# Kernel optimization log

Measured on AMD Instinct MI355X. Metric: run time of the kernel, lower is better.

The kernel has to match this reference:

```python
import jax, jax.numpy as jnp
import numpy as np

B = 8192
NUM_NODES = 100000
EMB = 128
W1D, W2D, W3D = 64, 128, 256   # witness_dims
CODE = 128
HID = 64                        # hardcoded hidden_dim in WitnessExtractor / decoder
TOTW = W1D + W2D + W3D          # 448


def _linear_params(key, fan_in, fan_out):
    k1, k2 = jax.random.split(key)
    bound = 1.0 / np.sqrt(fan_in)
    w = jax.random.uniform(k1, (fan_out, fan_in), jnp.float32, -bound, bound)
    b = jax.random.uniform(k2, (fan_out,), jnp.float32, -bound, bound)
    return w, b


def setup_inputs() -> dict:
    key = jax.random.key(0)
    ks = jax.random.split(key, 12)
    u = jax.random.randint(ks[0], (B,), 0, NUM_NODES, dtype=jnp.int64 if jax.config.jax_enable_x64 else jnp.int32)
    v = jax.random.randint(ks[1], (B,), 0, NUM_NODES, dtype=u.dtype)
    emb = jax.random.normal(ks[2], (NUM_NODES, EMB), jnp.float32)
    e1_w1, e1_b1 = _linear_params(ks[3], 2 * EMB, HID)
    e1_w2, e1_b2 = _linear_params(ks[4], HID, W1D)
    e2_w1, e2_b1 = _linear_params(ks[5], 2 * EMB + W1D, HID)
    e2_w2, e2_b2 = _linear_params(ks[6], HID, W2D)
    e3_w1, e3_b1 = _linear_params(ks[7], 2 * EMB + W2D, HID)
    e3_w2, e3_b2 = _linear_params(ks[8], HID, W3D)
    trop_w = jax.random.normal(ks[9], (CODE, TOTW), jnp.float32)  # init_scale=1.0
    dec_w1, dec_b1 = _linear_params(ks[10], CODE, HID)
    dec_w2, dec_b2 = _linear_params(ks[11], HID, 1)
    return dict(u=u, v=v, emb=emb,
                e1_w1=e1_w1, e1_b1=e1_b1, e1_w2=e1_w2, e1_b2=e1_b2,
                e2_w1=e2_w1, e2_b1=e2_b1, e2_w2=e2_w2, e2_b2=e2_b2,
                e3_w1=e3_w1, e3_b1=e3_b1, e3_w2=e3_w2, e3_b2=e3_b2,
                trop_w=trop_w, dec_w1=dec_w1, dec_b1=dec_b1,
                dec_w2=dec_w2, dec_b2=dec_b2)


def _witness(x, w1, b1, w2, b2):
    h = jax.nn.relu(x @ w1.T + b1)
    return jax.nn.sigmoid(h @ w2.T + b2)


def reference(u, v, emb,
              e1_w1, e1_b1, e1_w2, e1_b2,
              e2_w1, e2_b1, e2_w2, e2_b2,
              e3_w1, e3_b1, e3_w2, e3_b2,
              trop_w, dec_w1, dec_b1, dec_w2, dec_b2):
    u_emb = emb[u]                               # [B, EMB]
    v_emb = emb[v]
    base = jnp.concatenate([u_emb, v_emb], axis=1)  # [B, 2*EMB]
    w1 = _witness(base, e1_w1, e1_b1, e1_w2, e1_b2)
    w2 = _witness(jnp.concatenate([base, w1], axis=1), e2_w1, e2_b1, e2_w2, e2_b2)
    w3 = _witness(jnp.concatenate([base, w2], axis=1), e3_w1, e3_b1, e3_w2, e3_b2)
    wit = jnp.concatenate([w1, w2, w3], axis=1)  # [B, TOTW]
    # tropical (min-plus) matmul: code[b,o] = min_j (wit[b,j] + trop_w[o,j])
    code = jnp.min(wit[:, None, :] + trop_w[None, :, :], axis=2)  # [B, CODE]
    h = jax.nn.relu(code @ dec_w1.T + dec_b1)
    return h @ dec_w2.T + dec_b2                 # [B, 1]
```

## Files before the change

kernel.cpp:

```cpp
#include <hip/hip_runtime.h>
#include <hip/hip_fp16.h>
#include <math.h>

#define BATCH 8192
#define EMB 128
#define NTHREADS 1024
#define NWAVES 16
#define CH 136
#define SLOT 32

#define OFF_E1W1 0
#define OFF_E1W2 16384
#define OFF_E2W1 20480
#define OFF_E2W2 40960
#define OFF_E3W1 49152
#define OFF_E3W2 73728
#define OFF_DW1  90112
#define OFF_DW2  98304
#define W_DENSE  98368

typedef __attribute__((ext_vector_type(8))) _Float16 v8h;
typedef __attribute__((ext_vector_type(4))) float v4f;

struct Smem {
    union {
        _Float16 XB[2][32 * CH];
        _Float16 CODE[2][16 * CH];
    } U;
    _Float16 WC[2][56 * CH];
    _Float16 H[2][8 * CH];
};

__global__ __launch_bounds__(1024) void prep_kernel(
    const float* __restrict__ s0, const float* __restrict__ s1,
    const float* __restrict__ s2, const float* __restrict__ s3,
    const float* __restrict__ s4, const float* __restrict__ s5,
    const float* __restrict__ s6, const float* __restrict__ s7,
    const float* __restrict__ trop, _Float16* __restrict__ ws)
{
    const int b = blockIdx.x;
    const int tid = threadIdx.x;
    if (b < 25) {
        const int idx4 = (b * 1024 + tid) * 4;
        if (idx4 >= W_DENSE) return;
        const float* src; int off;
        if      (idx4 < OFF_E1W2) { src = s0; off = OFF_E1W1; }
        else if (idx4 < OFF_E2W1) { src = s1; off = OFF_E1W2; }
        else if (idx4 < OFF_E2W2) { src = s2; off = OFF_E2W1; }
        else if (idx4 < OFF_E3W1) { src = s3; off = OFF_E2W2; }
        else if (idx4 < OFF_E3W2) { src = s4; off = OFF_E3W1; }
        else if (idx4 < OFF_DW1)  { src = s5; off = OFF_E3W2; }
        else if (idx4 < OFF_DW2)  { src = s6; off = OFF_DW1;  }
        else                      { src = s7; off = OFF_DW2;  }
        const float4 v = *(const float4*)(src + (idx4 - off));
        _Float16* dst = ws + idx4;
        dst[0] = (_Float16)v.x; dst[1] = (_Float16)v.y;
        dst[2] = (_Float16)v.z; dst[3] = (_Float16)v.w;
    } else {
        const int lane = tid & 63;
        const int wave = tid >> 6;
        const int o = (b - 25) * 16 + wave;
        if (o >= 128) return;
        unsigned int* base = (unsigned int*)(ws + W_DENSE);

        const float* row = trop + (size_t)o * 448;
        float vals[7];
        float mn = 1e30f;
        #pragma unroll
        for (int it = 0; it < 7; ++it) {
            vals[it] = row[lane + it * 64];
            mn = fminf(mn, vals[it]);
        }
        mn = fminf(mn, __shfl_xor(mn, 1, 64));
        mn = fminf(mn, __shfl_xor(mn, 2, 64));
        mn = fminf(mn, __shfl_xor(mn, 4, 64));
        mn = fminf(mn, __shfl_xor(mn, 8, 64));
        mn = fminf(mn, __shfl_xor(mn, 16, 64));
        mn = fminf(mn, __shfl_xor(mn, 32, 64));
        const float thr = mn + 1.02f;

        const unsigned long long ltmask = (1ull << lane) - 1ull;
        unsigned int pos0 = 0;
        #pragma unroll
        for (int it = 0; it < 7; ++it) {
            const bool sel = vals[it] <= thr;
            const unsigned long long m = __ballot(sel);
            if (sel) {
                const unsigned int pos = pos0 + (unsigned)__popcll(m & ltmask);
                if (pos < SLOT) {
                    const unsigned short hb =
                        __builtin_bit_cast(unsigned short, (_Float16)vals[it]);
                    base[o * SLOT + pos] = ((unsigned)(lane + it * 64) << 16) | hb;
                }
            }
            pos0 += (unsigned)__popcll(m);
        }
        if (lane == 0) base[4096 + o] = pos0;
    }
}

template <int K, int O, int ACT>
__device__ __forceinline__ void dense_job(
    const _Float16* __restrict__ Wg, const float* __restrict__ bias,
    const _Float16* A0, _Float16* OutC, int jid, int lane)
{
    constexpr int STEPS = K / 32;
    static_assert(STEPS % 2 == 0, "even steps");
    const int l15 = lane & 15;
    const int quad = lane >> 4;
    const int o = jid * 16 + l15;
    const _Float16* wrow = Wg + (size_t)o * K + quad * 8;
    v4f c0 = {0.f, 0.f, 0.f, 0.f};
    v4f c1 = {0.f, 0.f, 0.f, 0.f};
    #pragma unroll
    for (int s = 0; s < STEPS; s += 2) {
        const v8h a0 = *(const v8h*)(A0 + (s * 4 + quad) * CH + l15 * 8);
        const v8h b0 = *(const v8h*)(wrow + s * 32);
        const v8h a1 = *(const v8h*)(A0 + ((s + 1) * 4 + quad) * CH + l15 * 8);
        const v8h b1 = *(const v8h*)(wrow + (s + 1) * 32);
        c0 = __builtin_amdgcn_mfma_f32_16x16x32_f16(a0, b0, c0, 0, 0, 0);
        c1 = __builtin_amdgcn_mfma_f32_16x16x32_f16(a1, b1, c1, 0, 0, 0);
    }
    const v4f c = c0 + c1;
    const float bs = bias[o];
    #pragma unroll
    for (int i = 0; i < 4; ++i) {
        float vv = c[i] + bs;
        if (ACT == 0) vv = fmaxf(vv, 0.f);
        else          vv = 1.f / (1.f + __expf(-vv));
        OutC[(o >> 3) * CH + (quad * 4 + i) * 8 + (o & 7)] = (_Float16)vv;
    }
}

__device__ __forceinline__ v4f base_gemm(
    const _Float16* __restrict__ ws, const _Float16* XB, int tgt, int nt,
    int lane, const float* __restrict__ b1, const float* __restrict__ b2,
    const float* __restrict__ b3)
{
    const int l15 = lane & 15;
    const int quad = lane >> 4;
    const int o = nt * 16 + l15;
    const _Float16* wrow;
    const float* bias;
    if (tgt == 0)      { wrow = ws + OFF_E1W1 + (size_t)o * 256; bias = b1; }
    else if (tgt == 1) { wrow = ws + OFF_E2W1 + (size_t)o * 320; bias = b2; }
    else               { wrow = ws + OFF_E3W1 + (size_t)o * 384; bias = b3; }
    wrow += quad * 8;
    v4f c0 = {0.f, 0.f, 0.f, 0.f};
    v4f c1 = {0.f, 0.f, 0.f, 0.f};
    #pragma unroll
    for (int s = 0; s < 8; s += 2) {
        const v8h a0 = *(const v8h*)(XB + (s * 4 + quad) * CH + l15 * 8);
        const v8h b0 = *(const v8h*)(wrow + s * 32);
        const v8h a1 = *(const v8h*)(XB + ((s + 1) * 4 + quad) * CH + l15 * 8);
        const v8h b1v = *(const v8h*)(wrow + (s + 1) * 32);
        c0 = __builtin_amdgcn_mfma_f32_16x16x32_f16(a0, b0, c0, 0, 0, 0);
        c1 = __builtin_amdgcn_mfma_f32_16x16x32_f16(a1, b1v, c1, 0, 0, 0);
    }
    v4f c = c0 + c1;
    const float bs = bias[o];
    #pragma unroll
    for (int i = 0; i < 4; ++i) c[i] += bs;
    return c;
}

template <int KW, int RS>
__device__ __forceinline__ void addpb_job(
    const _Float16* __restrict__ Wg, const _Float16* A0,
    const v4f hold, _Float16* OutH, int jid, int lane)
{
    constexpr int STEPS = KW / 32;
    static_assert(STEPS % 2 == 0, "even steps");
    const int l15 = lane & 15;
    const int quad = lane >> 4;
    const int o = jid * 16 + l15;
    const _Float16* wrow = Wg + (size_t)o * RS + quad * 8;
    v4f c0 = hold;
    v4f c1 = {0.f, 0.f, 0.f, 0.f};
    #pragma unroll
    for (int s = 0; s < STEPS; s += 2) {
        const v8h a0 = *(const v8h*)(A0 + (s * 4 + quad) * CH + l15 * 8);
        const v8h b0 = *(const v8h*)(wrow + s * 32);
        const v8h a1 = *(const v8h*)(A0 + ((s + 1) * 4 + quad) * CH + l15 * 8);
        const v8h b1 = *(const v8h*)(wrow + (s + 1) * 32);
        c0 = __builtin_amdgcn_mfma_f32_16x16x32_f16(a0, b0, c0, 0, 0, 0);
        c1 = __builtin_amdgcn_mfma_f32_16x16x32_f16(a1, b1, c1, 0, 0, 0);
    }
    const v4f c = c0 + c1;
    #pragma unroll
    for (int i = 0; i < 4; ++i) {
        const float vv = fmaxf(c[i], 0.f);
        OutH[(o >> 3) * CH + (quad * 4 + i) * 8 + (o & 7)] = (_Float16)vv;
    }
}

__global__ __launch_bounds__(NTHREADS, 8) void tacit_fused_kernel(
    const int* __restrict__ u, const int* __restrict__ v,
    const float* __restrict__ emb,
    const float* __restrict__ e1_b1, const float* __restrict__ e1_b2,
    const float* __restrict__ e2_b1, const float* __restrict__ e2_b2,
    const float* __restrict__ e3_b1, const float* __restrict__ e3_b2,
    const float* __restrict__ dec_b1, const float* __restrict__ dec_b2,
    const float* __restrict__ trop,
    const _Float16* __restrict__ ws,
    float* __restrict__ out)
{
    __shared__ Smem S;
    const int tid = threadIdx.x;
    const int lane = tid & 63;
    const int wave = tid >> 6;
    const int row0 = blockIdx.x * 32;

    {
        const int t   = tid >> 9;
        const int t9  = tid & 511;
        const int row = t9 & 15;
        const int kq  = t9 >> 4;
        const int node = (kq < 16) ? u[row0 + t * 16 + row] : v[row0 + t * 16 + row];
        const int col = (kq & 15) * 8;
        const float4 f0 = *(const float4*)(emb + (size_t)node * EMB + col);
        const float4 f1 = *(const float4*)(emb + (size_t)node * EMB + col + 4);
        v8h hv;
        hv[0] = (_Float16)f0.x; hv[1] = (_Float16)f0.y;
        hv[2] = (_Float16)f0.z; hv[3] = (_Float16)f0.w;
        hv[4] = (_Float16)f1.x; hv[5] = (_Float16)f1.y;
        hv[6] = (_Float16)f1.z; hv[7] = (_Float16)f1.w;
        *(v8h*)&S.U.XB[t][kq * CH + row * 8] = hv;
    }
    __syncthreads();

    v4f hold_a = {0.f, 0.f, 0.f, 0.f};
    v4f hold_b = {0.f, 0.f, 0.f, 0.f};
    {
        const int l15 = lane & 15;
        const int quad = lane >> 4;
        if (wave < 12) {
            const int tgt = wave >> 2;
            const v4f c = base_gemm(ws, S.U.XB[0], tgt, wave & 3, lane,
                                    e1_b1, e2_b1, e3_b1);
            if (tgt == 0) {
                const int o = (wave & 3) * 16 + l15;
                #pragma unroll
                for (int i = 0; i < 4; ++i)
                    S.H[0][(o >> 3) * CH + (quad * 4 + i) * 8 + (o & 7)] =
                        (_Float16)fmaxf(c[i], 0.f);
            } else {
                hold_a = c;
            }
        } else {
            const v4f c = base_gemm(ws, S.U.XB[1], 0, wave & 3, lane,
                                    e1_b1, e2_b1, e3_b1);
            const int o = (wave & 3) * 16 + l15;
            #pragma unroll
            for (int i = 0; i < 4; ++i)
                S.H[1][(o >> 3) * CH + (quad * 4 + i) * 8 + (o & 7)] =
                    (_Float16)fmaxf(c[i], 0.f);
        }
        if (wave < 8) {
            hold_b = base_gemm(ws, S.U.XB[1], (wave >> 2) + 1, wave & 3, lane,
                               e1_b1, e2_b1, e3_b1);
        }
    }
    __syncthreads();

    if (wave >= 8)
        dense_job<64, 64, 1>(ws + OFF_E1W2, e1_b2, S.H[(wave - 8) >> 2],
                             S.WC[(wave - 8) >> 2], (wave - 8) & 3, lane);
    __syncthreads();

    if (wave >= 4 && wave < 8)
        addpb_job<64, 320>(ws + OFF_E2W1 + 256, S.WC[0], hold_a, S.H[0], wave - 4, lane);
    else if (wave < 4)
        addpb_job<64, 320>(ws + OFF_E2W1 + 256, S.WC[1], hold_b, S.H[1], wave, lane);
    __syncthreads();

    dense_job<64, 128, 1>(ws + OFF_E2W2, e2_b2, S.H[wave >> 3],
                          S.WC[wave >> 3] + 8 * CH, wave & 7, lane);
    __syncthreads();

    if (wave >= 8 && wave < 12)
        addpb_job<128, 384>(ws + OFF_E3W1 + 256, S.WC[0] + 8 * CH, hold_a,
                            S.H[0], wave - 8, lane);
    else if (wave >= 4 && wave < 8)
        addpb_job<128, 384>(ws + OFF_E3W1 + 256, S.WC[1] + 8 * CH, hold_b,
                            S.H[1], wave - 4, lane);
    __syncthreads();

    dense_job<64, 256, 1>(ws + OFF_E3W2, e3_b2, S.H[0], S.WC[0] + 24 * CH, wave, lane);
    dense_job<64, 256, 1>(ws + OFF_E3W2, e3_b2, S.H[1], S.WC[1] + 24 * CH, wave, lane);
    __syncthreads();

    {
        const unsigned int* entg = (const unsigned int*)(ws + W_DENSE);
        const unsigned int* cntg = entg + 4096;
        const int r = lane & 15;
        const int cp = lane >> 4;
        #pragma unroll 1
        for (int t = 0; t < 2; ++t) {
            const _Float16* wr8 = &S.WC[t][r * 8];
            float acc[8];
            int idx8[8], end8[8];
            #pragma unroll
            for (int i = 0; i < 8; ++i) {
                const int o = (wave << 3) + i;
                const int n = (int)cntg[o];
                idx8[i] = o * SLOT + cp;
                end8[i] = o * SLOT + (n < SLOT ? n : SLOT);
                acc[i] = 1e30f;
            }
            bool any = true;
            while (any) {
                any = false;
                #pragma unroll
                for (int i = 0; i < 8; ++i) {
                    if (idx8[i] < end8[i]) {
                        const unsigned int cwv = entg[idx8[i]];
                        const int j = (int)(cwv >> 16);
                        const float tv = (float)__builtin_bit_cast(
                            _Float16, (unsigned short)(cwv & 0xffffu));
                        acc[i] = fminf(acc[i], (float)wr8[(j >> 3) * CH + (j & 7)] + tv);
                        idx8[i] += 4;
                        any = true;
                    }
                }
            }
            #pragma unroll
            for (int i = 0; i < 8; ++i) {
                const int o = (wave << 3) + i;
                if ((int)cntg[o] > SLOT) {
                    const float* trow = trop + (size_t)o * 448;
                    for (int j = cp; j < 448; j += 4)
                        acc[i] = fminf(acc[i],
                                       (float)wr8[(j >> 3) * CH + (j & 7)] + trow[j]);
                }
            }
            #pragma unroll
            for (int i = 0; i < 8; ++i) {
                float a = acc[i];
                a = fminf(a, __shfl_xor(a, 16, 64));
                a = fminf(a, __shfl_xor(a, 32, 64));
                if (cp == 0) {
                    const int o = (wave << 3) + i;
                    S.U.CODE[t][(o >> 3) * CH + r * 8 + (o & 7)] = (_Float16)a;
                }
            }
        }
    }
    __syncthreads();

    if (wave < 8)
        dense_job<128, 64, 0>(ws + OFF_DW1, dec_b1, S.U.CODE[wave >> 2],
                              S.H[wave >> 2], wave & 3, lane);
    __syncthreads();

    if (wave < 2) {
        const int r = lane & 15;
        const int part = lane >> 4;
        const _Float16* w2 = ws + OFF_DW2;
        float s = 0.f;
        #pragma unroll
        for (int q = 0; q < 2; ++q) {
            const int c = part + q * 4;
            const v8h hr = *(const v8h*)(&S.H[wave][c * CH + r * 8]);
            const v8h wr = *(const v8h*)(w2 + c * 8);
            #pragma unroll
            for (int t = 0; t < 8; ++t) s += (float)hr[t] * (float)wr[t];
        }
        s += __shfl_xor(s, 16, 64);
        s += __shfl_xor(s, 32, 64);
        if (part == 0) out[row0 + wave * 16 + r] = s + dec_b2[0];
    }
}

extern "C" void kernel_launch(void* const* d_in, const int* in_sizes, int n_in,
                              void* d_out, int out_size, void* d_ws, size_t ws_size,
                              hipStream_t stream) {
    const int*   u      = (const int*)d_in[0];
    const int*   v      = (const int*)d_in[1];
    const float* emb    = (const float*)d_in[2];
    const float* e1_w1  = (const float*)d_in[3];
    const float* e1_b1  = (const float*)d_in[4];
    const float* e1_w2  = (const float*)d_in[5];
    const float* e1_b2  = (const float*)d_in[6];
    const float* e2_w1  = (const float*)d_in[7];
    const float* e2_b1  = (const float*)d_in[8];
    const float* e2_w2  = (const float*)d_in[9];
    const float* e2_b2  = (const float*)d_in[10];
    const float* e3_w1  = (const float*)d_in[11];
    const float* e3_b1  = (const float*)d_in[12];
    const float* e3_w2  = (const float*)d_in[13];
    const float* e3_b2  = (const float*)d_in[14];
    const float* trop_w = (const float*)d_in[15];
    const float* dec_w1 = (const float*)d_in[16];
    const float* dec_b1 = (const float*)d_in[17];
    const float* dec_w2 = (const float*)d_in[18];
    const float* dec_b2 = (const float*)d_in[19];
    float* out = (float*)d_out;
    _Float16* ws = (_Float16*)d_ws;

    prep_kernel<<<33, 1024, 0, stream>>>(
        e1_w1, e1_w2, e2_w1, e2_w2, e3_w1, e3_w2, dec_w1, dec_w2, trop_w, ws);

    tacit_fused_kernel<<<BATCH / 32, NTHREADS, 0, stream>>>(
        u, v, emb,
        e1_b1, e1_b2, e2_b1, e2_b2, e3_b1, e3_b2, dec_b1, dec_b2,
        trop_w, ws, out);
}
```

Measured before the change: 163.9 us.

## Shrink blocks to 8 rows with 512 threads for more parallelism

Restructures the fused kernel so each block handles 8 batch rows with 8 waves instead of 32 rows with 16 waves. The 16-row MFMA tile is zero-padded, and the wave-to-job assignment for each stage is remapped to a single tile. This launches 1024 blocks instead of 256, which gives better CU coverage and latency hiding. The cost is that half of every MFMA tile is wasted on padding and the weights are re-read by four times as many blocks.

Result: slower. 185.4 us (+13.1%).

```diff
diff --git a/kernel.cpp b/kernel.cpp
--- a/kernel.cpp
+++ b/kernel.cpp
@@ -4,8 +4,9 @@
 
 #define BATCH 8192
 #define EMB 128
-#define NTHREADS 1024
-#define NWAVES 16
+#define NTHREADS 512
+#define NWAVES 8
+#define ROWS 8
 #define CH 136
 #define SLOT 32
 
@@ -24,11 +25,11 @@
 
 struct Smem {
     union {
-        _Float16 XB[2][32 * CH];
-        _Float16 CODE[2][16 * CH];
+        _Float16 XB[32 * CH];
+        _Float16 CODE[16 * CH];
     } U;
-    _Float16 WC[2][56 * CH];
-    _Float16 H[2][8 * CH];
+    _Float16 WC[56 * CH];
+    _Float16 H[8 * CH];
 };
 
 __global__ __launch_bounds__(1024) void prep_kernel(
@@ -209,14 +210,12 @@
     const int tid = threadIdx.x;
     const int lane = tid & 63;
     const int wave = tid >> 6;
-    const int row0 = blockIdx.x * 32;
-
-    {
-        const int t   = tid >> 9;
-        const int t9  = tid & 511;
-        const int row = t9 & 15;
-        const int kq  = t9 >> 4;
-        const int node = (kq < 16) ? u[row0 + t * 16 + row] : v[row0 + t * 16 + row];
+    const int row0 = blockIdx.x * ROWS;
+
+    if (tid < 256) {
+        const int row = tid & 7;
+        const int kq = tid >> 3;
+        const int node = (kq < 16) ? u[row0 + row] : v[row0 + row];
         const int col = (kq & 15) * 8;
         const float4 f0 = *(const float4*)(emb + (size_t)node * EMB + col);
         const float4 f1 = *(const float4*)(emb + (size_t)node * EMB + col + 4);
@@ -225,69 +224,51 @@
         hv[2] = (_Float16)f0.z; hv[3] = (_Float16)f0.w;
         hv[4] = (_Float16)f1.x; hv[5] = (_Float16)f1.y;
         hv[6] = (_Float16)f1.z; hv[7] = (_Float16)f1.w;
-        *(v8h*)&S.U.XB[t][kq * CH + row * 8] = hv;
-    }
-    __syncthreads();
-
-    v4f hold_a = {0.f, 0.f, 0.f, 0.f};
-    v4f hold_b = {0.f, 0.f, 0.f, 0.f};
-    {
+        *(v8h*)&S.U.XB[kq * CH + row * 8] = hv;
+    } else {
+        const int t = tid - 256;
+        const int row = 8 + (t & 7);
+        const int kq = t >> 3;
+        v8h z = {(_Float16)0.f, (_Float16)0.f, (_Float16)0.f, (_Float16)0.f,
+                 (_Float16)0.f, (_Float16)0.f, (_Float16)0.f, (_Float16)0.f};
+        *(v8h*)&S.U.XB[kq * CH + row * 8] = z;
+    }
+    __syncthreads();
+
+    v4f hold2 = {0.f, 0.f, 0.f, 0.f};
+    v4f hold3 = {0.f, 0.f, 0.f, 0.f};
+    if (wave < 4) {
+        const v4f c = base_gemm(ws, S.U.XB, 0, wave, lane, e1_b1, e2_b1, e3_b1);
         const int l15 = lane & 15;
         const int quad = lane >> 4;
-        if (wave < 12) {
-            const int tgt = wave >> 2;
-            const v4f c = base_gemm(ws, S.U.XB[0], tgt, wave & 3, lane,
-                                    e1_b1, e2_b1, e3_b1);
-            if (tgt == 0) {
-                const int o = (wave & 3) * 16 + l15;
-                #pragma unroll
-                for (int i = 0; i < 4; ++i)
-                    S.H[0][(o >> 3) * CH + (quad * 4 + i) * 8 + (o & 7)] =
-                        (_Float16)fmaxf(c[i], 0.f);
-            } else {
-                hold_a = c;
-            }
-        } else {
-            const v4f c = base_gemm(ws, S.U.XB[1], 0, wave & 3, lane,
-                                    e1_b1, e2_b1, e3_b1);
-            const int o = (wave & 3) * 16 + l15;
-            #pragma unroll
-            for (int i = 0; i < 4; ++i)
-                S.H[1][(o >> 3) * CH + (quad * 4 + i) * 8 + (o & 7)] =
-                    (_Float16)fmaxf(c[i], 0.f);
-        }
-        if (wave < 8) {
-            hold_b = base_gemm(ws, S.U.XB[1], (wave >> 2) + 1, wave & 3, lane,
-                               e1_b1, e2_b1, e3_b1);
-        }
-    }
-    __syncthreads();
-
-    if (wave >= 8)
-        dense_job<64, 64, 1>(ws + OFF_E1W2, e1_b2, S.H[(wave - 8) >> 2],
-                             S.WC[(wave - 8) >> 2], (wave - 8) & 3, lane);
-    __syncthreads();
-
-    if (wave >= 4 && wave < 8)
-        addpb_job<64, 320>(ws + OFF_E2W1 + 256, S.WC[0], hold_a, S.H[0], wave - 4, lane);
-    else if (wave < 4)
-        addpb_job<64, 320>(ws + OFF_E2W1 + 256, S.WC[1], hold_b, S.H[1], wave, lane);
-    __syncthreads();
-
-    dense_job<64, 128, 1>(ws + OFF_E2W2, e2_b2, S.H[wave >> 3],
-                          S.WC[wave >> 3] + 8 * CH, wave & 7, lane);
-    __syncthreads();
-
-    if (wave >= 8 && wave < 12)
-        addpb_job<128, 384>(ws + OFF_E3W1 + 256, S.WC[0] + 8 * CH, hold_a,
-                            S.H[0], wave - 8, lane);
-    else if (wave >= 4 && wave < 8)
-        addpb_job<128, 384>(ws + OFF_E3W1 + 256, S.WC[1] + 8 * CH, hold_b,
-                            S.H[1], wave - 4, lane);
-    __syncthreads();
-
-    dense_job<64, 256, 1>(ws + OFF_E3W2, e3_b2, S.H[0], S.WC[0] + 24 * CH, wave, lane);
-    dense_job<64, 256, 1>(ws + OFF_E3W2, e3_b2, S.H[1], S.WC[1] + 24 * CH, wave, lane);
+        const int o = wave * 16 + l15;
+        #pragma unroll
+        for (int i = 0; i < 4; ++i)
+            S.H[(o >> 3) * CH + (quad * 4 + i) * 8 + (o & 7)] =
+                (_Float16)fmaxf(c[i], 0.f);
+        hold3 = base_gemm(ws, S.U.XB, 2, wave, lane, e1_b1, e2_b1, e3_b1);
+    } else {
+        hold2 = base_gemm(ws, S.U.XB, 1, wave - 4, lane, e1_b1, e2_b1, e3_b1);
+    }
+    __syncthreads();
+
+    if (wave >= 4)
+        dense_job<64, 64, 1>(ws + OFF_E1W2, e1_b2, S.H, S.WC, wave - 4, lane);
+    __syncthreads();
+
+    if (wave >= 4)
+        addpb_job<64, 320>(ws + OFF_E2W1 + 256, S.WC, hold2, S.H, wave - 4, lane);
+    __syncthreads();
+
+    dense_job<64, 128, 1>(ws + OFF_E2W2, e2_b2, S.H, S.WC + 8 * CH, wave, lane);
+    __syncthreads();
+
+    if (wave < 4)
+        addpb_job<128, 384>(ws + OFF_E3W1 + 256, S.WC + 8 * CH, hold3, S.H, wave, lane);
+    __syncthreads();
+
+    dense_job<64, 256, 1>(ws + OFF_E3W2, e3_b2, S.H, S.WC + 24 * CH, wave, lane);
+    dense_job<64, 256, 1>(ws + OFF_E3W2, e3_b2, S.H, S.WC + 24 * CH, wave + 8, lane);
     __syncthreads();
 
     {
@@ -295,14 +276,15 @@
         const unsigned int* cntg = entg + 4096;
         const int r = lane & 15;
         const int cp = lane >> 4;
+        const _Float16* wr8 = &S.WC[r * 8];
         #pragma unroll 1
-        for (int t = 0; t < 2; ++t) {
-            const _Float16* wr8 = &S.WC[t][r * 8];
+        for (int oo = 0; oo < 2; ++oo) {
+            const int ob = wave * 16 + oo * 8;
             float acc[8];
             int idx8[8], end8[8];
             #pragma unroll
             for (int i = 0; i < 8; ++i) {
-                const int o = (wave << 3) + i;
+                const int o = ob + i;
                 const int n = (int)cntg[o];
                 idx8[i] = o * SLOT + cp;
                 end8[i] = o * SLOT + (n < SLOT ? n : SLOT);
@@ -326,7 +308,7 @@
             }
             #pragma unroll
             for (int i = 0; i < 8; ++i) {
-                const int o = (wave << 3) + i;
+                const int o = ob + i;
                 if ((int)cntg[o] > SLOT) {
                     const float* trow = trop + (size_t)o * 448;
                     for (int j = cp; j < 448; j += 4)
@@ -340,20 +322,19 @@
                 a = fminf(a, __shfl_xor(a, 16, 64));
                 a = fminf(a, __shfl_xor(a, 32, 64));
                 if (cp == 0) {
-                    const int o = (wave << 3) + i;
-                    S.U.CODE[t][(o >> 3) * CH + r * 8 + (o & 7)] = (_Float16)a;
+                    const int o = ob + i;
+                    S.U.CODE[(o >> 3) * CH + r * 8 + (o & 7)] = (_Float16)a;
                 }
             }
         }
     }
     __syncthreads();
 
-    if (wave < 8)
-        dense_job<128, 64, 0>(ws + OFF_DW1, dec_b1, S.U.CODE[wave >> 2],
-                              S.H[wave >> 2], wave & 3, lane);
-    __syncthreads();
-
-    if (wave < 2) {
+    if (wave >= 4)
+        dense_job<128, 64, 0>(ws + OFF_DW1, dec_b1, S.U.CODE, S.H, wave - 4, lane);
+    __syncthreads();
+
+    if (tid < 64) {
         const int r = lane & 15;
         const int part = lane >> 4;
         const _Float16* w2 = ws + OFF_DW2;
@@ -361,14 +342,14 @@
         #pragma unroll
         for (int q = 0; q < 2; ++q) {
             const int c = part + q * 4;
-            const v8h hr = *(const v8h*)(&S.H[wave][c * CH + r * 8]);
+            const v8h hr = *(const v8h*)(&S.H[c * CH + r * 8]);
             const v8h wr = *(const v8h*)(w2 + c * 8);
             #pragma unroll
             for (int t = 0; t < 8; ++t) s += (float)hr[t] * (float)wr[t];
         }
         s += __shfl_xor(s, 16, 64);
         s += __shfl_xor(s, 32, 64);
-        if (part == 0) out[row0 + wave * 16 + r] = s + dec_b2[0];
+        if (part == 0 && r < ROWS) out[row0 + r] = s + dec_b2[0];
     }
 }
 
@@ -401,7 +382,7 @@
     prep_kernel<<<33, 1024, 0, stream>>>(
         e1_w1, e1_w2, e2_w1, e2_w2, e3_w1, e3_w2, dec_w1, dec_w2, trop_w, ws);
 
-    tacit_fused_kernel<<<BATCH / 32, NTHREADS, 0, stream>>>(
+    tacit_fused_kernel<<<BATCH / ROWS, NTHREADS, 0, stream>>>(
         u, v, emb,
         e1_b1, e1_b2, e2_b1, e2_b2, e3_b1, e3_b2, dec_b1, dec_b2,
         trop_w, ws, out);
```
